# Kernel tuning notes

Measured on AMD Instinct MI355X. Metric: run time of the kernel, lower is better.

The kernel has to match this reference:

```python
import jax, jax.numpy as jnp
import numpy as np

N, E, C, H, IN = 100000, 800000, 47, 128, 128
ALPHA, THETA, RSL = 0.1, 0.5, 0.5
L = 4


def setup_inputs() -> dict:
    key = jax.random.key(0)
    ks = jax.random.split(key, 11)
    x = jax.random.normal(ks[0], (N, IN), jnp.float32)
    edge_index = jax.random.randint(ks[1], (2, E), 0, N, dtype=jnp.int32)
    edge_weight = jax.random.uniform(ks[2], (E,), jnp.float32)
    label = jax.random.randint(ks[3], (N,), 0, C, dtype=jnp.int32)
    p = jax.random.uniform(ks[4], (N, C), jnp.float32)
    cm = jax.random.normal(ks[5], (C, 1, C), jnp.float32)
    lin0_w = jax.random.normal(ks[6], (IN, H), jnp.float32) * 0.05
    lin0_b = jnp.zeros((H,), jnp.float32)
    lin1_w = jax.random.normal(ks[7], (H, C), jnp.float32) * 0.05
    lin1_b = jnp.zeros((C,), jnp.float32)
    conv_w = jax.random.normal(ks[8], (L, H, H), jnp.float32) * 0.05  # glorot-ish scale
    return {"x": x, "edge_index": edge_index, "edge_weight": edge_weight,
            "label": label, "p": p, "cm": cm,
            "lin0_w": lin0_w, "lin0_b": lin0_b,
            "lin1_w": lin1_w, "lin1_b": lin1_b, "conv_w": conv_w}


def _gcn2_forward(x, edge_index, edge_weight, label, p, cm,
                  lin0_w, lin0_b, lin1_w, lin1_b, conv_w):
    src, dst = edge_index[0], edge_index[1]
    # input linear + relu (dropout p=0 -> identity)
    x = jax.nn.relu(x @ lin0_w + lin0_b)
    x0 = x
    ones_n = jnp.ones((N,), x.dtype)
    for i in range(L):
        beta = float(np.log(THETA / (i + 1) + 1.0))
        # sparse propagate: sum_j edge_weight_ij * x_j  (aggr='add')
        msgs = x[src] * edge_weight[:, None]          # [E, H]
        out = jax.ops.segment_sum(msgs, dst, num_segments=N)  # [N, H]
        # --- RSL branch (rsl > 0) ---
        s = x + 0.1 * x0
        sums = jax.ops.segment_sum(s, label, num_segments=C)       # [C, H]
        cnt = jax.ops.segment_sum(ones_n, label, num_segments=C)   # [C]
        centers = jax.lax.stop_gradient(sums / jnp.maximum(cnt, 1.0)[:, None])
        r = centers[:, None, :] - centers[None, :, :]  # [C, C, H], r[i,j]=c_i-c_j
        rn = jnp.linalg.norm(r, axis=-1, keepdims=True)
        rn = jnp.where(rn == 0, jnp.ones_like(rn), rn)
        r = r / rn
        r = jnp.matmul(cm, r).squeeze(1)  # [C,1,C] @ [C,C,H] -> [C,1,H] -> [C,H]
        r = p @ r                         # [N, H]
        a = out - x
        out = x + RSL * r + (1.0 - RSL) * a
        # identity mapping + initial residual (shared_weights=True)
        out = out * (1.0 - ALPHA) + ALPHA * x0
        out = (1.0 - beta) * out + beta * (out @ conv_w[i])
        x = jax.nn.relu(out)
    return x @ lin1_w + lin1_b  # [N, C]


def reference(x, edge_index, edge_weight, label, p, cm,
              lin0_w, lin0_b, lin1_w, lin1_b, conv_w):
    return _gcn2_forward(x, edge_index, edge_weight, label, p, cm,
                         lin0_w, lin0_b, lin1_w, lin1_b, conv_w)
```

## Files before the change

### kernel.cpp

```cpp
#include <hip/hip_runtime.h>
#include <math.h>

#define NN 100000
#define EE 800000
#define CC 47
#define HH 128
#define NB 391
#define CHUNK 2000
#define CH (CC * HH)

typedef __attribute__((ext_vector_type(8))) short short8v;
typedef __attribute__((ext_vector_type(4))) float float4v;

__device__ inline ushort f2bf(float f) {
    unsigned u = __float_as_uint(f);
    unsigned r = (u + 0x7fffu + ((u >> 16) & 1u)) >> 16;
    return (ushort)r;
}
__device__ inline float b2f(ushort u) { return __uint_as_float(((unsigned)u) << 16); }

__global__ __launch_bounds__(256) void zero_kernel(int* __restrict__ z, int n) {
    for (int i = blockIdx.x * 256 + threadIdx.x; i < n; i += gridDim.x * 256) z[i] = 0;
}

__global__ __launch_bounds__(256) void hist_kernel(const int* __restrict__ dst,
                                                   int* __restrict__ deg, int e) {
    int i = blockIdx.x * 256 + threadIdx.x;
    if (i < e) atomicAdd(&deg[dst[i]], 1);
}

__global__ __launch_bounds__(256) void scan_block_kernel(const int* __restrict__ deg,
                                                         int* __restrict__ rowptr,
                                                         int* __restrict__ bsum, int n) {
    __shared__ int ls[256];
    int b = blockIdx.x, t = threadIdx.x;
    int i0 = b * 512 + 2 * t;
    int a0 = (i0 < n) ? deg[i0] : 0;
    int a1 = (i0 + 1 < n) ? deg[i0 + 1] : 0;
    int val = a0 + a1;
    ls[t] = val;
    __syncthreads();
    for (int off = 1; off < 256; off <<= 1) {
        int add = (t >= off) ? ls[t - off] : 0;
        __syncthreads();
        val += add;
        ls[t] = val;
        __syncthreads();
    }
    int incl1 = val;
    int incl0 = val - a1;
    if (i0 < n) rowptr[i0 + 1] = incl0;
    if (i0 + 1 < n) rowptr[i0 + 2] = incl1;
    if (t == 255) bsum[b] = val;
}

__global__ __launch_bounds__(256) void scan_bsum_kernel(int* __restrict__ bsum, int nb) {
    __shared__ int ls[256];
    int t = threadIdx.x;
    int v = (t < nb) ? bsum[t] : 0;
    int orig = v;
    ls[t] = v;
    __syncthreads();
    for (int off = 1; off < 256; off <<= 1) {
        int add = (t >= off) ? ls[t - off] : 0;
        __syncthreads();
        v += add;
        ls[t] = v;
        __syncthreads();
    }
    if (t < nb) bsum[t] = v - orig;
}

__global__ __launch_bounds__(256) void add_off_kernel(int* __restrict__ rowptr,
                                                      const int* __restrict__ bsum, int n) {
    int i = blockIdx.x * 256 + threadIdx.x;
    if (i < n) rowptr[i + 1] += bsum[i >> 9];
    if (i == 0) rowptr[0] = 0;
}

__global__ __launch_bounds__(256) void init_bcur_kernel(const int* __restrict__ rowptr,
                                                        int* __restrict__ bcur) {
    int b = blockIdx.x * 256 + threadIdx.x;
    if (b < 512) bcur[b] = rowptr[min(b * 256, NN)];
}

__global__ __launch_bounds__(256) void coarse_fill_kernel(const int* __restrict__ src,
                                                          const int* __restrict__ dst,
                                                          const float* __restrict__ ew,
                                                          int* __restrict__ bcur,
                                                          int2* __restrict__ stage, int e) {
    __shared__ int hist[512];
    __shared__ int base_local[512];
    __shared__ int gbase[512];
    __shared__ int lc[512];
    __shared__ int ls[256];
    __shared__ int2 le[CHUNK];
    __shared__ ushort lb[CHUNK];
    int t = threadIdx.x;
    int beg = blockIdx.x * CHUNK, end = min(e, beg + CHUNK);
    int cnt = end - beg;
    for (int i = t; i < 512; i += 256) { hist[i] = 0; lc[i] = 0; }
    __syncthreads();
    for (int i = beg + t; i < end; i += 256) atomicAdd(&hist[((unsigned)dst[i]) >> 8], 1);
    __syncthreads();
    int a0 = hist[2 * t], a1 = hist[2 * t + 1];
    int val = a0 + a1;
    ls[t] = val;
    __syncthreads();
    for (int off = 1; off < 256; off <<= 1) {
        int add = (t >= off) ? ls[t - off] : 0;
        __syncthreads();
        val += add;
        ls[t] = val;
        __syncthreads();
    }
    base_local[2 * t] = val - a0 - a1;
    base_local[2 * t + 1] = val - a1;
    __syncthreads();
    for (int b = t; b < 512; b += 256)
        if (hist[b] > 0) gbase[b] = atomicAdd(&bcur[b], hist[b]);
    __syncthreads();
    for (int i = beg + t; i < end; i += 256) {
        int d = dst[i];
        int bk = ((unsigned)d) >> 8;
        int slot = base_local[bk] + atomicAdd(&lc[bk], 1);
        le[slot] = make_int2(((d & 255) << 24) | src[i], __float_as_int(ew[i]));
        lb[slot] = (ushort)bk;
    }
    __syncthreads();
    for (int s = t; s < cnt; s += 256) {
        int bk = lb[s];
        stage[gbase[bk] + (s - base_local[bk])] = le[s];
    }
}

__global__ __launch_bounds__(256) void fine_fill_kernel(const int2* __restrict__ stage,
                                                        const int* __restrict__ rowptr,
                                                        int2* __restrict__ csr, int n) {
    __shared__ int cur[256];
    __shared__ int rp[257];
    int b = blockIdx.x, t = threadIdx.x;
    int node0 = b * 256;
    int nodes = min(256, n - node0);
    cur[t] = 0;
    rp[t] = rowptr[min(node0 + t, n)];
    if (t == 0) rp[256] = rowptr[min(node0 + 256, n)];
    __syncthreads();
    int S = rp[0], E = rp[nodes];
    for (int i = S + t; i < E; i += 256) {
        int2 en = stage[i];
        int dl = ((unsigned)en.x) >> 24;
        int pos = rp[dl] + atomicAdd(&cur[dl], 1);
        csr[pos] = make_int2(en.x & 0xFFFFFF, en.y);
    }
}

__global__ __launch_bounds__(256) void lhist_kernel(const int* __restrict__ label,
                                                    int* __restrict__ lcnt, int n) {
    __shared__ int lh[CC];
    if (threadIdx.x < CC) lh[threadIdx.x] = 0;
    __syncthreads();
    for (int i = blockIdx.x * 256 + threadIdx.x; i < n; i += gridDim.x * 256)
        atomicAdd(&lh[label[i]], 1);
    __syncthreads();
    if (threadIdx.x < CC) atomicAdd(&lcnt[threadIdx.x], lh[threadIdx.x]);
}

__global__ __launch_bounds__(64) void lscan_kernel(const int* __restrict__ lcnt,
                                                   int* __restrict__ lbase,
                                                   int* __restrict__ gcur,
                                                   float* __restrict__ cntf) {
    __shared__ int ls[CC];
    int t = threadIdx.x;
    if (t < CC) {
        int v = lcnt[t];
        cntf[t] = (float)v;
        gcur[t] = 0;
        ls[t] = v;
    }
    __syncthreads();
    if (t == 0) {
        int run = 0;
        for (int c = 0; c < CC; c++) { int x = ls[c]; ls[c] = run; run += x; }
    }
    __syncthreads();
    if (t < CC) lbase[t] = ls[t];
}

__global__ __launch_bounds__(256) void lfill_kernel(const int* __restrict__ label,
                                                    const int* __restrict__ lbase,
                                                    int* __restrict__ gcur,
                                                    int* __restrict__ perm, int n) {
    __shared__ int lh[CC], lbs[CC], lc[CC];
    int t = threadIdx.x;
    if (t < CC) lh[t] = 0;
    __syncthreads();
    int chunk = (n + gridDim.x - 1) / gridDim.x;
    int beg = blockIdx.x * chunk, end = min(n, beg + chunk);
    for (int i = beg + t; i < end; i += 256) atomicAdd(&lh[label[i]], 1);
    __syncthreads();
    if (t < CC) {
        lbs[t] = (lh[t] > 0) ? atomicAdd(&gcur[t], lh[t]) : 0;
        lc[t] = 0;
    }
    __syncthreads();
    for (int i = beg + t; i < end; i += 256) {
        int c = label[i];
        int pos = atomicAdd(&lc[c], 1);
        perm[lbase[c] + lbs[c] + pos] = (c << 24) | i;
    }
}

__global__ __launch_bounds__(256) void psum_kernel(const ushort* __restrict__ xb,
                                                   const int* __restrict__ perm,
                                                   float* __restrict__ sums, int n) {
    const int lane = threadIdx.x & 63;
    const int wid = threadIdx.x >> 6;
    int gw = blockIdx.x * 4 + wid;
    int nw = gridDim.x * 4;
    int per = (n + nw - 1) / nw;
    int beg = gw * per, end = min(n, beg + per);
    if (beg >= end) return;
    float ax = 0.0f, ay = 0.0f;
    int ccur = __builtin_amdgcn_readfirstlane(perm[beg]) >> 24;
    int i = beg;
    while (i < end) {
        if (i + 4 <= end) {
            int p0 = __builtin_amdgcn_readfirstlane(perm[i]);
            int p1 = __builtin_amdgcn_readfirstlane(perm[i + 1]);
            int p2 = __builtin_amdgcn_readfirstlane(perm[i + 2]);
            int p3 = __builtin_amdgcn_readfirstlane(perm[i + 3]);
            if ((p0 >> 24) == (p3 >> 24)) {
                int c = p0 >> 24;
                if (c != ccur) {
                    atomicAdd(&sums[ccur * HH + 2 * lane], ax);
                    atomicAdd(&sums[ccur * HH + 2 * lane + 1], ay);
                    ax = ay = 0.0f;
                    ccur = c;
                }
                ushort2 v0 = *(const ushort2*)(xb + (size_t)(p0 & 0xFFFFFF) * HH + 2 * lane);
                ushort2 v1 = *(const ushort2*)(xb + (size_t)(p1 & 0xFFFFFF) * HH + 2 * lane);
                ushort2 v2 = *(const ushort2*)(xb + (size_t)(p2 & 0xFFFFFF) * HH + 2 * lane);
                ushort2 v3 = *(const ushort2*)(xb + (size_t)(p3 & 0xFFFFFF) * HH + 2 * lane);
                ax += b2f(v0.x) + b2f(v1.x) + b2f(v2.x) + b2f(v3.x);
                ay += b2f(v0.y) + b2f(v1.y) + b2f(v2.y) + b2f(v3.y);
                i += 4;
                continue;
            }
        }
        int pe = __builtin_amdgcn_readfirstlane(perm[i]);
        int c = pe >> 24;
        if (c != ccur) {
            atomicAdd(&sums[ccur * HH + 2 * lane], ax);
            atomicAdd(&sums[ccur * HH + 2 * lane + 1], ay);
            ax = ay = 0.0f;
            ccur = c;
        }
        ushort2 v = *(const ushort2*)(xb + (size_t)(pe & 0xFFFFFF) * HH + 2 * lane);
        ax += b2f(v.x);
        ay += b2f(v.y);
        i += 1;
    }
    atomicAdd(&sums[ccur * HH + 2 * lane], ax);
    atomicAdd(&sums[ccur * HH + 2 * lane + 1], ay);
}

__global__ __launch_bounds__(256) void pack_all_kernel(const float* __restrict__ lin0_w,
                                                       const float* __restrict__ conv_w,
                                                       const float* __restrict__ W1,
                                                       ushort* __restrict__ wp0,
                                                       ushort* __restrict__ wpc,
                                                       ushort* __restrict__ wp1) {
    int idx = blockIdx.x * 256 + threadIdx.x;
    if (idx < 5 * 16384) {
        int m = idx >> 14;
        int r = idx & 16383;
        int k = r >> 7, c = r & 127;
        const float* W = (m == 0) ? lin0_w : conv_w + (size_t)(m - 1) * 16384;
        ushort* Wp = (m == 0) ? wp0 : wpc + (size_t)(m - 1) * 16384;
        Wp[(k >> 3) * 1024 + c * 8 + (k & 7)] = f2bf(W[r]);
    } else {
        int j = idx - 5 * 16384;
        if (j < 6144) {
            int ksub = j / 384, rem = j - ksub * 384;
            int c = rem >> 3, kk = ksub * 8 + (rem & 7);
            wp1[j] = (c < CC) ? f2bf(W1[kk * CC + c]) : (ushort)0;
        }
    }
}

__global__ __launch_bounds__(256) void lin0_mfma_kernel(const float* __restrict__ xin,
                                                        const ushort* __restrict__ Wp,
                                                        const float* __restrict__ bias,
                                                        ushort* __restrict__ x0b,
                                                        ushort* __restrict__ xb) {
    __shared__ ushort ts[32 * 128];
    const int lane = threadIdx.x & 63, wv = threadIdx.x >> 6;
    const int sub = lane >> 4, r16 = lane & 15;
    const int wbase = wv * 32;
    const int rowbase = blockIdx.x * 32;
    const float* tp = xin + (size_t)rowbase * HH;
    #pragma unroll
    for (int j = 0; j < 4; j++) {
        int e = 4 * threadIdx.x + j * 1024;
        float4 f = *(const float4*)(tp + e);
        int r = e >> 7, c = e & 127;
        ushort4 b4 = make_ushort4(f2bf(f.x), f2bf(f.y), f2bf(f.z), f2bf(f.w));
        int off = (r * 256 + c * 2) ^ ((r & 7) << 4);
        *(ushort4*)((char*)ts + off) = b4;
    }
    __syncthreads();
    float4v acc[2][2] = {};
    {
        const char* tsc = (const char*)ts;
        const int sw = (r16 & 7) << 4;
        #pragma unroll
        for (int ks = 0; ks < 4; ks++) {
            short8v a0 = *(const short8v*)(tsc + ((r16 * 256 + ks * 64 + sub * 16) ^ sw));
            short8v a1 = *(const short8v*)(tsc + (((16 + r16) * 256 + ks * 64 + sub * 16) ^ sw));
            int kb = (ks * 4 + sub) * 1024;
            short8v b0 = *(const short8v*)(Wp + kb + (wbase + r16) * 8);
            short8v b1 = *(const short8v*)(Wp + kb + (wbase + 16 + r16) * 8);
            acc[0][0] = __builtin_amdgcn_mfma_f32_16x16x32_bf16(a0, b0, acc[0][0], 0, 0, 0);
            acc[0][1] = __builtin_amdgcn_mfma_f32_16x16x32_bf16(a0, b1, acc[0][1], 0, 0, 0);
            acc[1][0] = __builtin_amdgcn_mfma_f32_16x16x32_bf16(a1, b0, acc[1][0], 0, 0, 0);
            acc[1][1] = __builtin_amdgcn_mfma_f32_16x16x32_bf16(a1, b1, acc[1][1], 0, 0, 0);
        }
    }
    float bv[2] = {bias[wbase + r16], bias[wbase + 16 + r16]};
    #pragma unroll
    for (int mi = 0; mi < 2; mi++)
        #pragma unroll
        for (int ni = 0; ni < 2; ni++) {
            int col = wbase + ni * 16 + r16;
            #pragma unroll
            for (int r = 0; r < 4; r++) {
                int row = rowbase + mi * 16 + sub * 4 + r;
                float v = fmaxf(acc[mi][ni][r] + bv[ni], 0.0f);
                ushort bv16 = f2bf(v);
                x0b[(size_t)row * HH + col] = bv16;
                xb[(size_t)row * HH + col] = bv16;
            }
        }
}

__global__ __launch_bounds__(64) void cr_kernel(const float* __restrict__ sumsx,
                                                const float* __restrict__ sums0,
                                                const float* __restrict__ cnt,
                                                const float* __restrict__ cm,
                                                ushort* __restrict__ rlp) {
    __shared__ float cs[CC * HH];
    int i = blockIdx.x, lane = threadIdx.x;
    for (int idx = lane; idx < CC * HH; idx += 64) {
        int c = idx >> 7;
        cs[idx] = (sumsx[idx] + 0.1f * sums0[idx]) / fmaxf(cnt[c], 1.0f);
    }
    __syncthreads();
    float ci0 = cs[i * HH + lane];
    float ci1 = cs[i * HH + 64 + lane];
    float acc0 = 0.0f, acc1 = 0.0f;
    for (int j = 0; j < CC; j++) {
        float d0 = ci0 - cs[j * HH + lane];
        float d1 = ci1 - cs[j * HH + 64 + lane];
        float s = d0 * d0 + d1 * d1;
        #pragma unroll
        for (int off = 32; off >= 1; off >>= 1) s += __shfl_xor(s, off);
        float nrm = sqrtf(s);
        if (nrm == 0.0f) nrm = 1.0f;
        float w = cm[i * CC + j] / nrm;
        acc0 = fmaf(w, d0, acc0);
        acc1 = fmaf(w, d1, acc1);
    }
    rlp[(i >> 3) * 1024 + lane * 8 + (i & 7)] = f2bf(acc0);
    rlp[(i >> 3) * 1024 + (lane + 64) * 8 + (i & 7)] = f2bf(acc1);
}

template <int FINAL>
__global__ __launch_bounds__(512, 8) void layer_kernel(
    const ushort* __restrict__ xin, const ushort* __restrict__ x0b,
    const float* __restrict__ p, const ushort* __restrict__ rlp,
    const int* __restrict__ rowptr, const int2* __restrict__ csr,
    const ushort* __restrict__ Wp,
    const ushort* __restrict__ Wp1, const float* __restrict__ b1,
    ushort* __restrict__ xout, float* __restrict__ out, float beta) {
    __shared__ ushort ts[32 * 128];
    __shared__ ushort ps[32 * 64];
    __shared__ ushort prs[32 * 128];
    const int lane = threadIdx.x & 63;
    const int wv = __builtin_amdgcn_readfirstlane(threadIdx.x >> 6);
    const int rowbase = blockIdx.x * 32;
    const int sub = lane >> 4, r16 = lane & 15;
    const int sw = (r16 & 7) << 4;
    if (threadIdx.x < 256) {
        int t = threadIdx.x;
        int r = t >> 3, kc = (t & 7) * 8;
        const float* prow = p + (size_t)(rowbase + r) * CC;
        short8v v;
        #pragma unroll
        for (int j = 0; j < 8; j++) {
            int k = kc + j;
            v[j] = (short)((k < CC) ? f2bf(prow[k]) : (ushort)0);
        }
        int off = (r * 128 + kc * 2) ^ ((r & 7) << 4);
        *(short8v*)((char*)ps + off) = v;
    }
    __syncthreads();
    {
        const char* psc = (const char*)ps;
        float4v pacc[2] = {};
        #pragma unroll
        for (int ks = 0; ks < 2; ks++) {
            short8v a0 = *(const short8v*)(psc + ((r16 * 128 + ks * 64 + sub * 16) ^ sw));
            short8v a1 = *(const short8v*)(psc + (((16 + r16) * 128 + ks * 64 + sub * 16) ^ sw));
            short8v bb = *(const short8v*)(rlp + (ks * 4 + sub) * 1024 + (16 * wv + r16) * 8);
            pacc[0] = __builtin_amdgcn_mfma_f32_16x16x32_bf16(a0, bb, pacc[0], 0, 0, 0);
            pacc[1] = __builtin_amdgcn_mfma_f32_16x16x32_bf16(a1, bb, pacc[1], 0, 0, 0);
        }
        int col = 16 * wv + r16;
        #pragma unroll
        for (int mi = 0; mi < 2; mi++)
            #pragma unroll
            for (int r = 0; r < 4; r++) {
                int rl_ = mi * 16 + sub * 4 + r;
                *(ushort*)((char*)prs + ((rl_ * 256 + col * 2) ^ ((rl_ & 7) << 4))) =
                    f2bf(pacc[mi][r]);
            }
    }
    __syncthreads();
    const int nn0 = rowbase + 4 * wv;
    int rp0 = __builtin_amdgcn_readfirstlane(rowptr[nn0]);
    int rp1 = __builtin_amdgcn_readfirstlane(rowptr[nn0 + 1]);
    int rp2 = __builtin_amdgcn_readfirstlane(rowptr[nn0 + 2]);
    int rp3 = __builtin_amdgcn_readfirstlane(rowptr[nn0 + 3]);
    int rp4 = __builtin_amdgcn_readfirstlane(rowptr[nn0 + 4]);
    float ax0 = 0, ay0 = 0, ax1 = 0, ay1 = 0, ax2 = 0, ay2 = 0, ax3 = 0, ay3 = 0;
#define ACC_EDGE(IDX, W, FX, FY)                                          \
    if ((IDX) < rp1) { ax0 = fmaf(W, FX, ax0); ay0 = fmaf(W, FY, ay0); }  \
    else if ((IDX) < rp2) { ax1 = fmaf(W, FX, ax1); ay1 = fmaf(W, FY, ay1); } \
    else if ((IDX) < rp3) { ax2 = fmaf(W, FX, ax2); ay2 = fmaf(W, FY, ay2); } \
    else { ax3 = fmaf(W, FX, ax3); ay3 = fmaf(W, FY, ay3); }
    int e2 = rp0;
    for (; e2 + 8 <= rp4; e2 += 8) {
        int2 ed[8];
        #pragma unroll
        for (int u = 0; u < 8; u++) ed[u] = csr[e2 + u];
        ushort2 vv[8];
        #pragma unroll
        for (int u = 0; u < 8; u++)
            vv[u] = *(const ushort2*)(xin + (size_t)ed[u].x * HH + 2 * lane);
        #pragma unroll
        for (int u = 0; u < 8; u++) {
            float w = __int_as_float(ed[u].y);
            float fx = b2f(vv[u].x), fy = b2f(vv[u].y);
            ACC_EDGE(e2 + u, w, fx, fy)
        }
    }
    for (; e2 < rp4; e2++) {
        int2 ed = csr[e2];
        ushort2 v = *(const ushort2*)(xin + (size_t)ed.x * HH + 2 * lane);
        float w = __int_as_float(ed.y);
        float fx = b2f(v.x), fy = b2f(v.y);
        ACC_EDGE(e2, w, fx, fy)
    }
#undef ACC_EDGE
    {
        float axs[4] = {ax0, ax1, ax2, ax3};
        float ays[4] = {ay0, ay1, ay2, ay3};
        #pragma unroll
        for (int k = 0; k < 4; k++) {
            int rloc = 4 * wv + k;
            int nn = nn0 + k;
            int poff = (rloc * 256 + lane * 4) ^ ((rloc & 7) << 4);
            ushort2 pv = *(const ushort2*)((const char*)prs + poff);
            ushort2 xc = *(const ushort2*)(xin + (size_t)nn * HH + 2 * lane);
            ushort2 xo = *(const ushort2*)(x0b + (size_t)nn * HH + 2 * lane);
            ushort2 o;
            o.x = f2bf(0.45f * b2f(xc.x) + 0.45f * b2f(pv.x) + 0.45f * axs[k] + 0.1f * b2f(xo.x));
            o.y = f2bf(0.45f * b2f(xc.y) + 0.45f * b2f(pv.y) + 0.45f * ays[k] + 0.1f * b2f(xo.y));
            *(ushort2*)((char*)ts + poff) = o;
        }
    }
    __syncthreads();
    const char* tsc = (const char*)ts;
    float4v acc[2] = {};
    #pragma unroll
    for (int ks = 0; ks < 4; ks++) {
        short8v a0 = *(const short8v*)(tsc + ((r16 * 256 + ks * 64 + sub * 16) ^ sw));
        short8v a1 = *(const short8v*)(tsc + (((16 + r16) * 256 + ks * 64 + sub * 16) ^ sw));
        short8v bb = *(const short8v*)(Wp + (ks * 4 + sub) * 1024 + (16 * wv + r16) * 8);
        acc[0] = __builtin_amdgcn_mfma_f32_16x16x32_bf16(a0, bb, acc[0], 0, 0, 0);
        acc[1] = __builtin_amdgcn_mfma_f32_16x16x32_bf16(a1, bb, acc[1], 0, 0, 0);
    }
    const float omb = 1.0f - beta;
    const int col = 16 * wv + r16;
    if constexpr (!FINAL) {
        #pragma unroll
        for (int mi = 0; mi < 2; mi++)
            #pragma unroll
            for (int r = 0; r < 4; r++) {
                int rl_ = mi * 16 + sub * 4 + r;
                int toff = (rl_ * 256 + col * 2) ^ ((rl_ & 7) << 4);
                float tv = b2f(*(const ushort*)(tsc + toff));
                float v = fmaxf(omb * tv + beta * acc[mi][r], 0.0f);
                xout[(size_t)(rowbase + rl_) * HH + col] = f2bf(v);
            }
    } else {
        __syncthreads();
        #pragma unroll
        for (int mi = 0; mi < 2; mi++)
            #pragma unroll
            for (int r = 0; r < 4; r++) {
                int rl_ = mi * 16 + sub * 4 + r;
                int toff = (rl_ * 256 + col * 2) ^ ((rl_ & 7) << 4);
                ushort* slot = (ushort*)((char*)ts + toff);
                float tv = b2f(*slot);
                float v = fmaxf(omb * tv + beta * acc[mi][r], 0.0f);
                *slot = f2bf(v);
            }
        __syncthreads();
        if (wv < 3) {
            float4v a2[2] = {};
            #pragma unroll
            for (int ks = 0; ks < 4; ks++) {
                short8v a0 = *(const short8v*)(tsc + ((r16 * 256 + ks * 64 + sub * 16) ^ sw));
                short8v a1 = *(const short8v*)(tsc + (((16 + r16) * 256 + ks * 64 + sub * 16) ^ sw));
                short8v bb = *(const short8v*)(Wp1 + (ks * 4 + sub) * 384 + (wv * 16 + r16) * 8);
                a2[0] = __builtin_amdgcn_mfma_f32_16x16x32_bf16(a0, bb, a2[0], 0, 0, 0);
                a2[1] = __builtin_amdgcn_mfma_f32_16x16x32_bf16(a1, bb, a2[1], 0, 0, 0);
            }
            int col2 = wv * 16 + r16;
            if (col2 < CC) {
                float bias = b1[col2];
                #pragma unroll
                for (int mi = 0; mi < 2; mi++)
                    #pragma unroll
                    for (int r = 0; r < 4; r++) {
                        int row = rowbase + mi * 16 + sub * 4 + r;
                        out[(size_t)row * CC + col2] = a2[mi][r] + bias;
                    }
            }
        }
    }
}

extern "C" void kernel_launch(void* const* d_in, const int* in_sizes, int n_in,
                              void* d_out, int out_size, void* d_ws, size_t ws_size,
                              hipStream_t stream) {
    const float* x_in   = (const float*)d_in[0];
    const int*   ei     = (const int*)d_in[1];
    const float* ew     = (const float*)d_in[2];
    const int*   label  = (const int*)d_in[3];
    const float* p      = (const float*)d_in[4];
    const float* cm     = (const float*)d_in[5];
    const float* lin0_w = (const float*)d_in[6];
    const float* lin0_b = (const float*)d_in[7];
    const float* lin1_w = (const float*)d_in[8];
    const float* lin1_b = (const float*)d_in[9];
    const float* conv_w = (const float*)d_in[10];
    float* out = (float*)d_out;

    const int* src = ei;
    const int* dst = ei + EE;

    const size_t NH = (size_t)NN * HH;
    float* ws = (float*)d_ws;
    float* sums0  = ws;
    float* sumsxs = sums0 + CH;
    ushort* rlp   = (ushort*)(sumsxs + 3 * CH);
    int*   deg    = (int*)(rlp + 8192);
    int*   lcnt   = deg + NN;
    const int ZTOT = CH + 3 * CH + 4096 + NN + 64;
    float* cnt    = (float*)(lcnt + 64);
    int*   rowptr = (int*)(cnt + 64);
    int*   bsum   = rowptr + NN + 64;
    int*   bcur   = bsum + 256;
    int*   lbase  = bcur + 512;
    int*   gcur   = lbase + 64;
    int*   perm   = gcur + 64;
    int2*  csr    = (int2*)(perm + NN);
    int2*  stage  = csr + EE;
    ushort* x0b   = (ushort*)(stage + EE);
    ushort* xbA   = x0b + NH;
    ushort* xbB   = xbA + NH;
    ushort* wp0   = xbB + NH;
    ushort* wpc   = wp0 + 16384;
    ushort* wp1   = wpc + 4 * 16384;

    zero_kernel<<<512, 256, 0, stream>>>((int*)ws, ZTOT);

    hist_kernel<<<(EE + 255) / 256, 256, 0, stream>>>(dst, deg, EE);
    const int NBLK = (NN + 511) / 512;
    scan_block_kernel<<<NBLK, 256, 0, stream>>>(deg, rowptr, bsum, NN);
    scan_bsum_kernel<<<1, 256, 0, stream>>>(bsum, NBLK);
    add_off_kernel<<<(NN + 255) / 256, 256, 0, stream>>>(rowptr, bsum, NN);
    init_bcur_kernel<<<2, 256, 0, stream>>>(rowptr, bcur);
    coarse_fill_kernel<<<(EE + CHUNK - 1) / CHUNK, 256, 0, stream>>>(src, dst, ew, bcur, stage, EE);
    fine_fill_kernel<<<NB, 256, 0, stream>>>(stage, rowptr, csr, NN);

    lhist_kernel<<<256, 256, 0, stream>>>(label, lcnt, NN);
    lscan_kernel<<<1, 64, 0, stream>>>(lcnt, lbase, gcur, cnt);
    lfill_kernel<<<256, 256, 0, stream>>>(label, lbase, gcur, perm, NN);

    pack_all_kernel<<<(5 * 16384 + 6144 + 255) / 256, 256, 0, stream>>>(
        lin0_w, conv_w, lin1_w, wp0, wpc, wp1);

    lin0_mfma_kernel<<<NN / 32, 256, 0, stream>>>(x_in, wp0, lin0_b, x0b, xbA);

    psum_kernel<<<2048, 256, 0, stream>>>(x0b, perm, sums0, NN);

    const float betas[4] = {logf(0.5f / 1.0f + 1.0f), logf(0.5f / 2.0f + 1.0f),
                            logf(0.5f / 3.0f + 1.0f), logf(0.5f / 4.0f + 1.0f)};

    ushort* xin_b = xbA;
    ushort* xout_b = xbB;
    for (int i = 0; i < 4; i++) {
        if (i == 0) {
            cr_kernel<<<CC, 64, 0, stream>>>(sums0, sums0, cnt, cm, rlp);
        } else {
            float* sx = sumsxs + (size_t)(i - 1) * CH;
            psum_kernel<<<2048, 256, 0, stream>>>(xin_b, perm, sx, NN);
            cr_kernel<<<CC, 64, 0, stream>>>(sx, sums0, cnt, cm, rlp);
        }
        if (i < 3) {
            layer_kernel<0><<<NN / 32, 512, 0, stream>>>(xin_b, x0b, p, rlp, rowptr, csr,
                                                         wpc + (size_t)i * 16384, wp1, lin1_b,
                                                         xout_b, out, betas[i]);
            ushort* tmp = xin_b; xin_b = xout_b; xout_b = tmp;
        } else {
            layer_kernel<1><<<NN / 32, 512, 0, stream>>>(xin_b, x0b, p, rlp, rowptr, csr,
                                                         wpc + 3 * 16384, wp1, lin1_b,
                                                         xout_b, out, betas[3]);
        }
    }
}
```

Before: 527.2 us.

## Fuse setup kernels and process one node at a time in SpMM gather

Several small preprocessing launches are merged. Zeroing and weight packing become one kernel, the degree and label histograms share a kernel, the two scans share a kernel, and the rowptr offset step now also initialises bcur. This cuts the setup kernel count from about eleven launches to six. The propagate/layer kernel now walks the edges of each of its four nodes in turn, with each half-wave taking alternate edges and loading 4 bf16 features per lane. The halves are combined by a cross-half shuffle, replacing the per-edge branchy four-way accumulator select. This doubles edges in flight per load and drops branching, at the cost of a sequential per-node loop and a shuffle reduction.

```diff
diff --git a/kernel.cpp b/kernel.cpp
--- a/kernel.cpp
+++ b/kernel.cpp
@@ -8,6 +8,7 @@
 #define NB 391
 #define CHUNK 2000
 #define CH (CC * HH)
+#define PACKN (5 * 16384 + 6144)
 
 typedef __attribute__((ext_vector_type(8))) short short8v;
 typedef __attribute__((ext_vector_type(4))) float float4v;
@@ -19,14 +20,47 @@
 }
 __device__ inline float b2f(ushort u) { return __uint_as_float(((unsigned)u) << 16); }
 
-__global__ __launch_bounds__(256) void zero_kernel(int* __restrict__ z, int n) {
-    for (int i = blockIdx.x * 256 + threadIdx.x; i < n; i += gridDim.x * 256) z[i] = 0;
-}
-
-__global__ __launch_bounds__(256) void hist_kernel(const int* __restrict__ dst,
-                                                   int* __restrict__ deg, int e) {
-    int i = blockIdx.x * 256 + threadIdx.x;
+__global__ __launch_bounds__(256) void prep_kernel(const float* __restrict__ lin0_w,
+                                                   const float* __restrict__ conv_w,
+                                                   const float* __restrict__ W1,
+                                                   ushort* __restrict__ wp0,
+                                                   ushort* __restrict__ wpc,
+                                                   ushort* __restrict__ wp1,
+                                                   int* __restrict__ z, int ztot) {
+    int idx = blockIdx.x * 256 + threadIdx.x;
+    int stride = gridDim.x * 256;
+    for (int i = idx; i < ztot; i += stride) z[i] = 0;
+    for (int i = idx; i < PACKN; i += stride) {
+        if (i < 5 * 16384) {
+            int m = i >> 14;
+            int r = i & 16383;
+            int k = r >> 7, c = r & 127;
+            const float* W = (m == 0) ? lin0_w : conv_w + (size_t)(m - 1) * 16384;
+            ushort* Wp = (m == 0) ? wp0 : wpc + (size_t)(m - 1) * 16384;
+            Wp[(k >> 3) * 1024 + c * 8 + (k & 7)] = f2bf(W[r]);
+        } else {
+            int j = i - 5 * 16384;
+            int ksub = j / 384, rem = j - ksub * 384;
+            int c = rem >> 3, kk = ksub * 8 + (rem & 7);
+            wp1[j] = (c < CC) ? f2bf(W1[kk * CC + c]) : (ushort)0;
+        }
+    }
+}
+
+__global__ __launch_bounds__(256) void hist2_kernel(const int* __restrict__ dst,
+                                                    int* __restrict__ deg,
+                                                    const int* __restrict__ label,
+                                                    int* __restrict__ lcnt, int e, int n) {
+    __shared__ int lh[CC];
+    int t = threadIdx.x;
+    if (t < CC) lh[t] = 0;
+    __syncthreads();
+    int i = blockIdx.x * 256 + t;
     if (i < e) atomicAdd(&deg[dst[i]], 1);
+    bool has = blockIdx.x < (unsigned)((n + 255) / 256);
+    if (has && i < n) atomicAdd(&lh[label[i]], 1);
+    __syncthreads();
+    if (has && t < CC && lh[t] > 0) atomicAdd(&lcnt[t], lh[t]);
 }
 
 __global__ __launch_bounds__(256) void scan_block_kernel(const int* __restrict__ deg,
@@ -54,34 +88,56 @@
     if (t == 255) bsum[b] = val;
 }
 
-__global__ __launch_bounds__(256) void scan_bsum_kernel(int* __restrict__ bsum, int nb) {
-    __shared__ int ls[256];
-    int t = threadIdx.x;
-    int v = (t < nb) ? bsum[t] : 0;
-    int orig = v;
-    ls[t] = v;
-    __syncthreads();
-    for (int off = 1; off < 256; off <<= 1) {
-        int add = (t >= off) ? ls[t - off] : 0;
-        __syncthreads();
-        v += add;
+__global__ __launch_bounds__(256) void scan2_kernel(int* __restrict__ bsum, int nb,
+                                                    const int* __restrict__ lcnt,
+                                                    int* __restrict__ lbase,
+                                                    int* __restrict__ gcur,
+                                                    float* __restrict__ cntf) {
+    if (blockIdx.x == 0) {
+        __shared__ int ls[256];
+        int t = threadIdx.x;
+        int v = (t < nb) ? bsum[t] : 0;
+        int orig = v;
         ls[t] = v;
         __syncthreads();
-    }
-    if (t < nb) bsum[t] = v - orig;
-}
-
-__global__ __launch_bounds__(256) void add_off_kernel(int* __restrict__ rowptr,
-                                                      const int* __restrict__ bsum, int n) {
+        for (int off = 1; off < 256; off <<= 1) {
+            int add = (t >= off) ? ls[t - off] : 0;
+            __syncthreads();
+            v += add;
+            ls[t] = v;
+            __syncthreads();
+        }
+        if (t < nb) bsum[t] = v - orig;
+    } else {
+        __shared__ int ls[CC];
+        int t = threadIdx.x;
+        if (t < CC) {
+            int v = lcnt[t];
+            cntf[t] = (float)v;
+            gcur[t] = 0;
+            ls[t] = v;
+        }
+        __syncthreads();
+        if (t == 0) {
+            int run = 0;
+            for (int c = 0; c < CC; c++) { int x = ls[c]; ls[c] = run; run += x; }
+        }
+        __syncthreads();
+        if (t < CC) lbase[t] = ls[t];
+    }
+}
+
+__global__ __launch_bounds__(256) void addoff_init_kernel(int* __restrict__ rowptr,
+                                                          const int* __restrict__ bsum,
+                                                          int* __restrict__ bcur, int n) {
     int i = blockIdx.x * 256 + threadIdx.x;
-    if (i < n) rowptr[i + 1] += bsum[i >> 9];
-    if (i == 0) rowptr[0] = 0;
-}
-
-__global__ __launch_bounds__(256) void init_bcur_kernel(const int* __restrict__ rowptr,
-                                                        int* __restrict__ bcur) {
-    int b = blockIdx.x * 256 + threadIdx.x;
-    if (b < 512) bcur[b] = rowptr[min(b * 256, NN)];
+    if (i < n) {
+        int v = rowptr[i + 1] + bsum[i >> 9];
+        rowptr[i + 1] = v;
+        if (((i + 1) & 255) == 0 && ((i + 1) >> 8) < 512) bcur[(i + 1) >> 8] = v;
+    }
+    if (i == 0) { rowptr[0] = 0; bcur[0] = 0; }
+    if (i < 512 && i * 256 >= n) bcur[i] = EE;
 }
 
 __global__ __launch_bounds__(256) void coarse_fill_kernel(const int* __restrict__ src,
@@ -153,38 +209,6 @@
         int pos = rp[dl] + atomicAdd(&cur[dl], 1);
         csr[pos] = make_int2(en.x & 0xFFFFFF, en.y);
     }
-}
-
-__global__ __launch_bounds__(256) void lhist_kernel(const int* __restrict__ label,
-                                                    int* __restrict__ lcnt, int n) {
-    __shared__ int lh[CC];
-    if (threadIdx.x < CC) lh[threadIdx.x] = 0;
-    __syncthreads();
-    for (int i = blockIdx.x * 256 + threadIdx.x; i < n; i += gridDim.x * 256)
-        atomicAdd(&lh[label[i]], 1);
-    __syncthreads();
-    if (threadIdx.x < CC) atomicAdd(&lcnt[threadIdx.x], lh[threadIdx.x]);
-}
-
-__global__ __launch_bounds__(64) void lscan_kernel(const int* __restrict__ lcnt,
-                                                   int* __restrict__ lbase,
-                                                   int* __restrict__ gcur,
-                                                   float* __restrict__ cntf) {
-    __shared__ int ls[CC];
-    int t = threadIdx.x;
-    if (t < CC) {
-        int v = lcnt[t];
-        cntf[t] = (float)v;
-        gcur[t] = 0;
-        ls[t] = v;
-    }
-    __syncthreads();
-    if (t == 0) {
-        int run = 0;
-        for (int c = 0; c < CC; c++) { int x = ls[c]; ls[c] = run; run += x; }
-    }
-    __syncthreads();
-    if (t < CC) lbase[t] = ls[t];
 }
 
 __global__ __launch_bounds__(256) void lfill_kernel(const int* __restrict__ label,
@@ -265,30 +289,6 @@
     atomicAdd(&sums[ccur * HH + 2 * lane + 1], ay);
 }
 
-__global__ __launch_bounds__(256) void pack_all_kernel(const float* __restrict__ lin0_w,
-                                                       const float* __restrict__ conv_w,
-                                                       const float* __restrict__ W1,
-                                                       ushort* __restrict__ wp0,
-                                                       ushort* __restrict__ wpc,
-                                                       ushort* __restrict__ wp1) {
-    int idx = blockIdx.x * 256 + threadIdx.x;
-    if (idx < 5 * 16384) {
-        int m = idx >> 14;
-        int r = idx & 16383;
-        int k = r >> 7, c = r & 127;
-        const float* W = (m == 0) ? lin0_w : conv_w + (size_t)(m - 1) * 16384;
-        ushort* Wp = (m == 0) ? wp0 : wpc + (size_t)(m - 1) * 16384;
-        Wp[(k >> 3) * 1024 + c * 8 + (k & 7)] = f2bf(W[r]);
-    } else {
-        int j = idx - 5 * 16384;
-        if (j < 6144) {
-            int ksub = j / 384, rem = j - ksub * 384;
-            int c = rem >> 3, kk = ksub * 8 + (rem & 7);
-            wp1[j] = (c < CC) ? f2bf(W1[kk * CC + c]) : (ushort)0;
-        }
-    }
-}
-
 __global__ __launch_bounds__(256) void lin0_mfma_kernel(const float* __restrict__ xin,
                                                         const ushort* __restrict__ Wp,
                                                         const float* __restrict__ bias,
@@ -433,51 +433,62 @@
     int rp2 = __builtin_amdgcn_readfirstlane(rowptr[nn0 + 2]);
     int rp3 = __builtin_amdgcn_readfirstlane(rowptr[nn0 + 3]);
     int rp4 = __builtin_amdgcn_readfirstlane(rowptr[nn0 + 4]);
-    float ax0 = 0, ay0 = 0, ax1 = 0, ay1 = 0, ax2 = 0, ay2 = 0, ax3 = 0, ay3 = 0;
-#define ACC_EDGE(IDX, W, FX, FY)                                          \
-    if ((IDX) < rp1) { ax0 = fmaf(W, FX, ax0); ay0 = fmaf(W, FY, ay0); }  \
-    else if ((IDX) < rp2) { ax1 = fmaf(W, FX, ax1); ay1 = fmaf(W, FY, ay1); } \
-    else if ((IDX) < rp3) { ax2 = fmaf(W, FX, ax2); ay2 = fmaf(W, FY, ay2); } \
-    else { ax3 = fmaf(W, FX, ax3); ay3 = fmaf(W, FY, ay3); }
-    int e2 = rp0;
-    for (; e2 + 8 <= rp4; e2 += 8) {
-        int2 ed[8];
-        #pragma unroll
-        for (int u = 0; u < 8; u++) ed[u] = csr[e2 + u];
-        ushort2 vv[8];
-        #pragma unroll
-        for (int u = 0; u < 8; u++)
-            vv[u] = *(const ushort2*)(xin + (size_t)ed[u].x * HH + 2 * lane);
-        #pragma unroll
-        for (int u = 0; u < 8; u++) {
-            float w = __int_as_float(ed[u].y);
-            float fx = b2f(vv[u].x), fy = b2f(vv[u].y);
-            ACC_EDGE(e2 + u, w, fx, fy)
-        }
-    }
-    for (; e2 < rp4; e2++) {
-        int2 ed = csr[e2];
-        ushort2 v = *(const ushort2*)(xin + (size_t)ed.x * HH + 2 * lane);
-        float w = __int_as_float(ed.y);
-        float fx = b2f(v.x), fy = b2f(v.y);
-        ACC_EDGE(e2, w, fx, fy)
-    }
-#undef ACC_EDGE
-    {
-        float axs[4] = {ax0, ax1, ax2, ax3};
-        float ays[4] = {ay0, ay1, ay2, ay3};
-        #pragma unroll
-        for (int k = 0; k < 4; k++) {
-            int rloc = 4 * wv + k;
-            int nn = nn0 + k;
-            int poff = (rloc * 256 + lane * 4) ^ ((rloc & 7) << 4);
-            ushort2 pv = *(const ushort2*)((const char*)prs + poff);
-            ushort2 xc = *(const ushort2*)(xin + (size_t)nn * HH + 2 * lane);
-            ushort2 xo = *(const ushort2*)(x0b + (size_t)nn * HH + 2 * lane);
-            ushort2 o;
-            o.x = f2bf(0.45f * b2f(xc.x) + 0.45f * b2f(pv.x) + 0.45f * axs[k] + 0.1f * b2f(xo.x));
-            o.y = f2bf(0.45f * b2f(xc.y) + 0.45f * b2f(pv.y) + 0.45f * ays[k] + 0.1f * b2f(xo.y));
-            *(ushort2*)((char*)ts + poff) = o;
+    int rps[5] = {rp0, rp1, rp2, rp3, rp4};
+    const int half = lane >> 5;
+    const int li = lane & 31;
+    #pragma unroll 1
+    for (int k = 0; k < 4; k++) {
+        int rloc = 4 * wv + k;
+        int nn = nn0 + k;
+        int beg = rps[k], end = rps[k + 1];
+        float a0 = 0, a1 = 0, a2 = 0, a3 = 0;
+        int e2 = beg;
+        for (; e2 + 8 <= end; e2 += 8) {
+            int2 ed[8];
+            #pragma unroll
+            for (int u = 0; u < 8; u++) ed[u] = csr[e2 + u];
+            ushort4 vv[4];
+            #pragma unroll
+            for (int q = 0; q < 4; q++) {
+                int2 em = half ? ed[2 * q + 1] : ed[2 * q];
+                vv[q] = *(const ushort4*)(xin + (size_t)em.x * HH + 4 * li);
+            }
+            #pragma unroll
+            for (int q = 0; q < 4; q++) {
+                int2 em = half ? ed[2 * q + 1] : ed[2 * q];
+                float w = __int_as_float(em.y);
+                a0 = fmaf(w, b2f(vv[q].x), a0);
+                a1 = fmaf(w, b2f(vv[q].y), a1);
+                a2 = fmaf(w, b2f(vv[q].z), a2);
+                a3 = fmaf(w, b2f(vv[q].w), a3);
+            }
+        }
+        for (; e2 < end; e2 += 2) {
+            int2 edA = csr[e2];
+            int2 edB = (e2 + 1 < end) ? csr[e2 + 1] : make_int2(edA.x, 0);
+            int2 em = half ? edB : edA;
+            float w = __int_as_float(em.y);
+            ushort4 v = *(const ushort4*)(xin + (size_t)em.x * HH + 4 * li);
+            a0 = fmaf(w, b2f(v.x), a0);
+            a1 = fmaf(w, b2f(v.y), a1);
+            a2 = fmaf(w, b2f(v.z), a2);
+            a3 = fmaf(w, b2f(v.w), a3);
+        }
+        a0 += __shfl_xor(a0, 32);
+        a1 += __shfl_xor(a1, 32);
+        a2 += __shfl_xor(a2, 32);
+        a3 += __shfl_xor(a3, 32);
+        if (half == 0) {
+            int poff = (rloc * 256 + li * 8) ^ ((rloc & 7) << 4);
+            ushort4 pv = *(const ushort4*)((const char*)prs + poff);
+            ushort4 xc = *(const ushort4*)(xin + (size_t)nn * HH + 4 * li);
+            ushort4 xo = *(const ushort4*)(x0b + (size_t)nn * HH + 4 * li);
+            ushort4 o;
+            o.x = f2bf(0.45f * b2f(xc.x) + 0.45f * b2f(pv.x) + 0.45f * a0 + 0.1f * b2f(xo.x));
+            o.y = f2bf(0.45f * b2f(xc.y) + 0.45f * b2f(pv.y) + 0.45f * a1 + 0.1f * b2f(xo.y));
+            o.z = f2bf(0.45f * b2f(xc.z) + 0.45f * b2f(pv.z) + 0.45f * a2 + 0.1f * b2f(xo.z));
+            o.w = f2bf(0.45f * b2f(xc.w) + 0.45f * b2f(pv.w) + 0.45f * a3 + 0.1f * b2f(xo.w));
+            *(ushort4*)((char*)ts + poff) = o;
         }
     }
     __syncthreads();
@@ -586,23 +597,16 @@
     ushort* wpc   = wp0 + 16384;
     ushort* wp1   = wpc + 4 * 16384;
 
-    zero_kernel<<<512, 256, 0, stream>>>((int*)ws, ZTOT);
-
-    hist_kernel<<<(EE + 255) / 256, 256, 0, stream>>>(dst, deg, EE);
+    prep_kernel<<<512, 256, 0, stream>>>(lin0_w, conv_w, lin1_w, wp0, wpc, wp1, (int*)ws, ZTOT);
+
+    hist2_kernel<<<(EE + 255) / 256, 256, 0, stream>>>(dst, deg, label, lcnt, EE, NN);
     const int NBLK = (NN + 511) / 512;
     scan_block_kernel<<<NBLK, 256, 0, stream>>>(deg, rowptr, bsum, NN);
-    scan_bsum_kernel<<<1, 256, 0, stream>>>(bsum, NBLK);
-    add_off_kernel<<<(NN + 255) / 256, 256, 0, stream>>>(rowptr, bsum, NN);
-    init_bcur_kernel<<<2, 256, 0, stream>>>(rowptr, bcur);
+    scan2_kernel<<<2, 256, 0, stream>>>(bsum, NBLK, lcnt, lbase, gcur, cnt);
+    addoff_init_kernel<<<(NN + 255) / 256, 256, 0, stream>>>(rowptr, bsum, bcur, NN);
     coarse_fill_kernel<<<(EE + CHUNK - 1) / CHUNK, 256, 0, stream>>>(src, dst, ew, bcur, stage, EE);
     fine_fill_kernel<<<NB, 256, 0, stream>>>(stage, rowptr, csr, NN);
-
-    lhist_kernel<<<256, 256, 0, stream>>>(label, lcnt, NN);
-    lscan_kernel<<<1, 64, 0, stream>>>(lcnt, lbase, gcur, cnt);
     lfill_kernel<<<256, 256, 0, stream>>>(label, lbase, gcur, perm, NN);
-
-    pack_all_kernel<<<(5 * 16384 + 6144 + 255) / 256, 256, 0, stream>>>(
-        lin0_w, conv_w, lin1_w, wp0, wpc, wp1);
 
     lin0_mfma_kernel<<<NN / 32, 256, 0, stream>>>(x_in, wp0, lin0_b, x0b, xbA);
 
```

Result: slower. 643.6 us (+22.1%).
